# Performance work log

Measured on AMD Instinct MI355X. Metric: run time of the kernel, lower is better.

The kernel has to match this reference:

```python
import jax, jax.numpy as jnp
import numpy as np

B = 16384
N_NODES = 55
N = B * N_NODES
IN_CH = 13
HID = 32
MAX_NBR = 6
N_LAYERS = 5
E = 4 * N


def _sage(x, src, dst, wl, bl, wr, n):
    # PyG SAGEConv: out = lin_l(mean_j x_j) + lin_r(x_i); lin_l has bias, lin_r does not.
    msgs = x[src]                                                   # [E, d]
    agg = jax.ops.segment_sum(msgs, dst, num_segments=n)            # [N, d]
    cnt = jax.ops.segment_sum(jnp.ones((src.shape[0],), x.dtype), dst, num_segments=n)
    agg = agg / jnp.maximum(cnt, 1.0)[:, None]
    return agg @ wl + bl + x @ wr


def setup_inputs() -> dict:
    key = jax.random.key(0)
    ks = jax.random.split(key, 24)
    x = jax.random.normal(ks[0], (N, IN_CH), dtype=jnp.float32)
    # column -3 (index 10) is a binary neighbor mask: exactly MAX_NBR ones per graph
    u = jax.random.uniform(ks[1], (B, N_NODES))
    nbr_idx = jnp.argsort(u, axis=1)[:, :MAX_NBR]
    mask = jnp.zeros((B, N_NODES), jnp.float32).at[jnp.arange(B)[:, None], nbr_idx].set(1.0)
    x = x.at[:, IN_CH - 3].set(mask.reshape(-1))
    edge_index = jax.random.randint(ks[2], (2, E), 0, N, dtype=jnp.int64)
    shuffle_indices = jax.random.randint(ks[3], (B, MAX_NBR), 0, MAX_NBR, dtype=jnp.int64)
    s = 0.1
    wl0 = jax.random.normal(ks[4], (IN_CH, HID)) * s
    bl0 = jnp.zeros((HID,), jnp.float32)
    wr0 = jax.random.normal(ks[5], (IN_CH, HID)) * s
    wl = jax.random.normal(ks[6], (N_LAYERS - 1, HID, HID)) * s
    bl = jnp.zeros((N_LAYERS - 1, HID), jnp.float32)
    wr = jax.random.normal(ks[7], (N_LAYERS - 1, HID, HID)) * s
    wq = jax.random.normal(ks[8], (HID, HID)) * s
    bq = jnp.zeros((HID,), jnp.float32)
    wk = jax.random.normal(ks[9], (HID, HID)) * s
    bk = jnp.zeros((HID,), jnp.float32)
    wv = jax.random.normal(ks[10], (HID, HID)) * s
    bv = jnp.zeros((HID,), jnp.float32)
    wo = jax.random.normal(ks[11], (HID, HID)) * s
    bo = jnp.zeros((HID,), jnp.float32)
    w_fc = jax.random.normal(ks[12], (HID * MAX_NBR, MAX_NBR)) * s
    b_fc = jnp.zeros((MAX_NBR,), jnp.float32)
    return {"x": x, "edge_index": edge_index, "shuffle_indices": shuffle_indices,
            "wl0": wl0, "bl0": bl0, "wr0": wr0, "wl": wl, "bl": bl, "wr": wr,
            "wq": wq, "bq": bq, "wk": wk, "bk": bk, "wv": wv, "bv": bv,
            "wo": wo, "bo": bo, "w_fc": w_fc, "b_fc": b_fc}


def reference(x, edge_index, shuffle_indices, wl0, bl0, wr0, wl, bl, wr,
              wq, bq, wk, bk, wv, bv, wo, bo, w_fc, b_fc):
    n = x.shape[0]
    b = n // N_NODES
    src, dst = edge_index[0], edge_index[1]
    nbr_mask = x[:, IN_CH - 3].reshape(b, N_NODES)                  # [B, 55]

    h = jax.nn.selu(_sage(x, src, dst, wl0, bl0, wr0, n))
    jk = h
    for i in range(N_LAYERS - 1):
        h = jax.nn.selu(_sage(h, src, dst, wl[i], bl[i], wr[i], n))
        jk = jnp.maximum(jk, h)                                     # JumpingKnowledge('max')

    h = jax.nn.selu(jk)                                             # [N, HID]
    keys = h.reshape(b, N_NODES, HID)
    values = keys

    # dynamic neighbor gather: indices of mask==1 in ascending order, zero-padded to MAX_NBR
    order = jnp.argsort(-nbr_mask, axis=1, stable=True)[:, :MAX_NBR]  # [B, 6]
    barange = jnp.arange(b)[:, None]
    query = keys[barange, order]                                    # [B, 6, HID]
    valid = jnp.take_along_axis(nbr_mask, order, axis=1) > 0.5      # [B, 6] bool
    query = jnp.where(valid[..., None], query, 0.0)
    query = query[barange, shuffle_indices]                         # shuffled gather

    # single-head cross attention (head_dim = HID)
    Q = query @ wq + bq
    K = keys @ wk + bk
    V = values @ wv + bv
    scores = jnp.einsum('bqd,bkd->bqk', Q, K) / jnp.sqrt(jnp.float32(HID))
    attn = jax.nn.softmax(scores, axis=-1)
    out = jnp.einsum('bqk,bkd->bqd', attn, V) @ wo + bo             # [B, 6, HID]

    out = jax.nn.selu(out.reshape(b, HID * MAX_NBR))
    return out @ w_fc + b_fc                                        # [B, 6]
```

## Files before the change

### kernel.cpp

```cpp
#include <hip/hip_runtime.h>
#include <cstdint>
#include <cstddef>

#define NODES   55
#define BGRAPH  16384
#define NTOT    (BGRAPH*NODES)
#define INCH    13
#define HID     32
#define ETOT    (4*NTOT)
#define NPB     128
#define ECAP    768
#define ZN      NTOT

#define NBUCK   220
#define BSH     12
#define BMSK    4095
#define NBLK    2048
#define BCAP2   32
#define BINTH   256
#define BINGRP  (ETOT/4/NBLK)
#define OVFCAP  8192

#define ASTR    72
#define BSTR    72
#define ASTR0   40
#define WKV_OFF 9216

typedef _Float16 f16;
typedef _Float16 f16x4 __attribute__((ext_vector_type(4)));
typedef _Float16 f16x8 __attribute__((ext_vector_type(8)));
typedef float    f32x4 __attribute__((ext_vector_type(4)));

__device__ __forceinline__ float selu_f(float v){
  const float s  = 1.0507009873554805f;
  const float sa = 1.7580993408473766f;
  return v > 0.f ? s*v : sa*(__expf(v)-1.f);
}

__global__ __launch_bounds__(256) void k_pad(const float* __restrict__ x,
                                             float* __restrict__ xf,
                                             uint32_t* __restrict__ ha32,
                                             int* __restrict__ ocnt){
  if (blockIdx.x == 0){
    int t = threadIdx.x;
    if (t == 0) *ocnt = 0;
    if (t < 16)            xf[(size_t)ZN*16 + t] = 0.f;
    if (t >= 16 && t < 32) ha32[(size_t)ZN*16 + (t-16)] = 0u;
  }
  int i = blockIdx.x*256 + threadIdx.x;
  int node = i>>2, q = i&3;
  const float* r = x + (size_t)node*INCH + q*4;
  float4 v;
  v.x = r[0];
  v.y = (q<3) ? r[1] : 0.f;
  v.z = (q<3) ? r[2] : 0.f;
  v.w = (q<3) ? r[3] : 0.f;
  ((float4*)xf)[i] = v;
}

__global__ __launch_bounds__(256) void k_wprep(
    const float* __restrict__ wl0, const float* __restrict__ wr0,
    const float* __restrict__ wl,  const float* __restrict__ wr,
    const float* __restrict__ wk,  const float* __restrict__ wv,
    f16* __restrict__ wcp)
{
  int t = threadIdx.x;
  for (int i=t; i<1024; i+=256){
    int oc = i>>5, k = i&31;
    float v = 0.f;
    if (k < 13)                 v = wl0[k*HID + oc];
    else if (k >= 16 && k < 29) v = wr0[(k-16)*HID + oc];
    wcp[oc*32 + k] = (f16)v;
  }
  for (int i=t; i<4*2048; i+=256){
    int l = i>>11, r = i&2047, oc = r>>6, k = r&63;
    float v = (k<32) ? wl[l*1024 + k*HID + oc] : wr[l*1024 + (k-32)*HID + oc];
    wcp[1024 + l*2048 + oc*64 + k] = (f16)v;
  }
  for (int i=t; i<2048; i+=256){
    int oc = i>>5, k = i&31;
    float v = (oc < 32) ? wk[k*HID + oc] : wv[k*HID + (oc-32)];
    wcp[WKV_OFF + oc*32 + k] = (f16)v;
  }
}

__global__ __launch_bounds__(BINTH) void k_bin(
    const int* __restrict__ src, const int* __restrict__ dst,
    uint32_t* __restrict__ binned, int* __restrict__ gcnt,
    uint2* __restrict__ ovf, int* __restrict__ ocnt)
{
  __shared__ int lcnt[NBUCK];
  int t = threadIdx.x, bid = blockIdx.x;
  for (int i=t;i<NBUCK;i+=BINTH) lcnt[i]=0;
  __syncthreads();
  const int4* s4 = (const int4*)src;
  const int4* d4 = (const int4*)dst;
  int g0 = bid*BINGRP;
  for (int i=t; i<BINGRP; i+=BINTH){
    int4 s = s4[g0+i];
    int4 d = d4[g0+i];
    #pragma unroll
    for (int j=0;j<4;j++){
      int dd = (&d.x)[j];
      int ss = (&s.x)[j];
      int b  = dd >> BSH;
      uint32_t entry = (uint32_t)ss | ((uint32_t)(dd & BMSK) << 20);
      int pos = atomicAdd(&lcnt[b], 1);
      if (pos < BCAP2) binned[((size_t)b*NBLK + bid)*BCAP2 + pos] = entry;
      else {
        int gp = atomicAdd(ocnt, 1);
        if (gp < OVFCAP) ovf[gp] = make_uint2(entry, (uint32_t)b);
      }
    }
  }
  __syncthreads();
  for (int i=t;i<NBUCK;i+=BINTH){
    int c = lcnt[i]; if (c > BCAP2) c = BCAP2;
    gcnt[bid*NBUCK + i] = c;
  }
}

__global__ __launch_bounds__(256) void k_btot(const int* __restrict__ gcnt,
                                              const uint2* __restrict__ ovf,
                                              const int* __restrict__ ocnt,
                                              int* __restrict__ btot){
  __shared__ int sd[256];
  int b = blockIdx.x, t = threadIdx.x;
  int s = 0;
  for (int i=t;i<NBLK;i+=256) s += gcnt[i*NBUCK + b];
  int oc = *ocnt; if (oc > OVFCAP) oc = OVFCAP;
  for (int j=t;j<oc;j+=256) if (ovf[j].y == (uint32_t)b) s++;
  sd[t]=s; __syncthreads();
  for (int o=128;o>0;o>>=1){ if (t<o) sd[t]+=sd[t+o]; __syncthreads(); }
  if (t==0) btot[b]=sd[0];
}

__global__ __launch_bounds__(256) void k_bscan(const int* __restrict__ btot,
                                               int* __restrict__ bbase){
  __shared__ int sd[256];
  int t = threadIdx.x;
  int v = (t<NBUCK) ? btot[t] : 0;
  sd[t] = v; __syncthreads();
  for (int o=1;o<256;o<<=1){
    int u = (t>=o) ? sd[t-o] : 0;
    __syncthreads();
    sd[t] += u;
    __syncthreads();
  }
  if (t<NBUCK) bbase[t] = sd[t] - v;
}

__global__ __launch_bounds__(1024) void k_bucket(
    const uint32_t* __restrict__ binned, const int* __restrict__ gcnt,
    const int* __restrict__ bbase,
    const uint2* __restrict__ ovf, const int* __restrict__ ocnt,
    int* __restrict__ off, uint32_t* __restrict__ csrp)
{
  __shared__ int hist[4096];
  __shared__ int cnts[NBLK];
  __shared__ int ws[1024];
  int b = blockIdx.x, t = threadIdx.x;
  int base = bbase[b];
  for (int i=t;i<NBLK;i+=1024) cnts[i] = gcnt[i*NBUCK + b];
  #pragma unroll
  for (int i=0;i<4;i++) hist[t+1024*i] = 0;
  int oc = *ocnt; if (oc > OVFCAP) oc = OVFCAP;
  __syncthreads();

  const uint4* bb4 = (const uint4*)(binned + (size_t)b*(NBLK*BCAP2));
  for (int i=t; i<NBLK*BCAP2/4; i+=1024){
    uint4 e = bb4[i];
    int c = cnts[i>>3];
    int s0 = (i&7)*4;
    if (s0   < c) atomicAdd(&hist[(e.x>>20)&BMSK],1);
    if (s0+1 < c) atomicAdd(&hist[(e.y>>20)&BMSK],1);
    if (s0+2 < c) atomicAdd(&hist[(e.z>>20)&BMSK],1);
    if (s0+3 < c) atomicAdd(&hist[(e.w>>20)&BMSK],1);
  }
  for (int j=t;j<oc;j+=1024){
    uint2 pr = ovf[j];
    if (pr.y == (uint32_t)b) atomicAdd(&hist[(pr.x>>20)&BMSK],1);
  }
  __syncthreads();
  int t4 = t*4;
  int s0=hist[t4], s1=hist[t4+1], s2=hist[t4+2], s3=hist[t4+3];
  int sum = s0+s1+s2+s3;
  ws[t] = sum; __syncthreads();
  for (int o=1;o<1024;o<<=1){
    int u = (t>=o) ? ws[t-o] : 0;
    __syncthreads();
    ws[t] += u;
    __syncthreads();
  }
  int ex = ws[t] - sum;
  int p0 = ex, p1 = ex+s0, p2 = ex+s0+s1, p3 = ex+s0+s1+s2;
  hist[t4]=p0; hist[t4+1]=p1; hist[t4+2]=p2; hist[t4+3]=p3;
  int4 ov; ov.x = base+p0; ov.y = base+p1; ov.z = base+p2; ov.w = base+p3;
  ((int4*)(off + (b<<BSH)))[t] = ov;
  if (b == NBUCK-1 && t == 1023) off[NTOT] = ETOT;
  __syncthreads();
  for (int i=t; i<NBLK*BCAP2/4; i+=1024){
    uint4 e = bb4[i];
    int c = cnts[i>>3];
    int s0b = (i&7)*4;
    int p;
    if (s0b   < c){ p = atomicAdd(&hist[(e.x>>20)&BMSK],1); csrp[base+p] = e.x & 0xFFFFFu; }
    if (s0b+1 < c){ p = atomicAdd(&hist[(e.y>>20)&BMSK],1); csrp[base+p] = e.y & 0xFFFFFu; }
    if (s0b+2 < c){ p = atomicAdd(&hist[(e.z>>20)&BMSK],1); csrp[base+p] = e.z & 0xFFFFFu; }
    if (s0b+3 < c){ p = atomicAdd(&hist[(e.w>>20)&BMSK],1); csrp[base+p] = e.w & 0xFFFFFu; }
  }
  for (int j=t;j<oc;j+=1024){
    uint2 pr = ovf[j];
    if (pr.y == (uint32_t)b){
      int p = atomicAdd(&hist[(pr.x>>20)&BMSK],1);
      csrp[base+p] = pr.x & 0xFFFFFu;
    }
  }
}

__global__ __launch_bounds__(256,8) void k_layer0(
    const float* __restrict__ xf,
    const int* __restrict__ off, const uint32_t* __restrict__ csrp,
    const f16* __restrict__ wcat0, const float* __restrict__ bl0,
    f16* __restrict__ hout)
{
  __shared__ uint32_t ALDS[NPB*(ASTR0/2)];
  __shared__ uint32_t BLDS[32*(ASTR0/2)];
  __shared__ uint32_t EL[ECAP];
  __shared__ int      sOFF[NPB+2];
  __shared__ float    biasL[32];
  int t = threadIdx.x;
  int base = blockIdx.x*NPB;
  int e0 = off[base];
  int e1 = off[base+NPB];
  for (int i=t; i<NPB+1; i+=256) sOFF[i] = off[base+i];
  {
    int lim = (e1-e0) < ECAP ? (e1-e0) : ECAP;
    for (int i=t; i<lim; i+=256) EL[i] = csrp[e0+i];
  }
  if (t < 128){
    int oc = t>>2, kq = (t&3)*8;
    f16x8 wv = *(const f16x8*)(wcat0 + oc*32 + kq);
    *(f16x8*)((f16*)BLDS + oc*ASTR0 + kq) = wv;
  }
  if (t < 32) biasL[t] = bl0[t];
  __syncthreads();

  int c4 = t & 3;
  #pragma unroll
  for (int p=0;p<2;p++){
    int nl = p*64 + (t>>2);
    int node = base + nl;
    float4 xown = *((const float4*)(xf + (size_t)node*16) + c4);
    int s = sOFF[nl] - e0;
    int d = sOFF[nl+1] - sOFF[nl];
    float a0=0.f,a1=0.f,a2=0.f,a3=0.f;
    for (int i=0;i<d;i+=4){
      int j0 = s+i;
      uint32_t k0,k1,k2,k3;
      if (j0+3 < ECAP){ k0=EL[j0]; k1=EL[j0+1]; k2=EL[j0+2]; k3=EL[j0+3]; }
      else            { k0=csrp[e0+j0]; k1=csrp[e0+j0+1]; k2=csrp[e0+j0+2]; k3=csrp[e0+j0+3]; }
      k1 = (i+1<d)?k1:(uint32_t)ZN;
      k2 = (i+2<d)?k2:(uint32_t)ZN;
      k3 = (i+3<d)?k3:(uint32_t)ZN;
      float4 g0 = *((const float4*)(xf + (size_t)k0*16u) + c4);
      float4 g1 = *((const float4*)(xf + (size_t)k1*16u) + c4);
      float4 g2 = *((const float4*)(xf + (size_t)k2*16u) + c4);
      float4 g3 = *((const float4*)(xf + (size_t)k3*16u) + c4);
      a0 += (g0.x+g1.x)+(g2.x+g3.x);
      a1 += (g0.y+g1.y)+(g2.y+g3.y);
      a2 += (g0.z+g1.z)+(g2.z+g3.z);
      a3 += (g0.w+g1.w)+(g2.w+g3.w);
    }
    float inv = 1.f/(float)(d<1?1:d);
    union { f16 h[4]; uint32_t u[2]; } mp, xp;
    mp.h[0]=(f16)(a0*inv); mp.h[1]=(f16)(a1*inv); mp.h[2]=(f16)(a2*inv); mp.h[3]=(f16)(a3*inv);
    xp.h[0]=(f16)xown.x;   xp.h[1]=(f16)xown.y;   xp.h[2]=(f16)xown.z;   xp.h[3]=(f16)xown.w;
    uint32_t* arow = &ALDS[nl*(ASTR0/2)];
    *((uint2*)&arow[2*c4])     = make_uint2(mp.u[0], mp.u[1]);
    *((uint2*)&arow[8 + 2*c4]) = make_uint2(xp.u[0], xp.u[1]);
  }
  __syncthreads();

  int w = t>>6, l = t&63;
  int lrow = l&15, lg = l>>4;
  const f16* Af = (const f16*)ALDS;
  const f16* Bf = (const f16*)BLDS;
  f32x4 D00={0.f,0.f,0.f,0.f}, D01=D00, D10=D00, D11=D00;
  {
    f16x8 af0 = *(const f16x8*)(Af + (32*w+lrow)*ASTR0    + 8*lg);
    f16x8 af1 = *(const f16x8*)(Af + (32*w+16+lrow)*ASTR0 + 8*lg);
    f16x8 bf0 = *(const f16x8*)(Bf + lrow*ASTR0           + 8*lg);
    f16x8 bf1 = *(const f16x8*)(Bf + (16+lrow)*ASTR0      + 8*lg);
    D00 = __builtin_amdgcn_mfma_f32_16x16x32_f16(af0, bf0, D00, 0,0,0);
    D01 = __builtin_amdgcn_mfma_f32_16x16x32_f16(af0, bf1, D01, 0,0,0);
    D10 = __builtin_amdgcn_mfma_f32_16x16x32_f16(af1, bf0, D10, 0,0,0);
    D11 = __builtin_amdgcn_mfma_f32_16x16x32_f16(af1, bf1, D11, 0,0,0);
  }
  __syncthreads();

  f16* ST = (f16*)ALDS;
  #pragma unroll
  for (int j=0;j<4;j++){
    int r0 = 32*w + 4*lg + j, r1 = r0 + 16;
    ST[r0*34 + lrow]      = (f16)selu_f(D00[j] + biasL[lrow]);
    ST[r0*34 + 16 + lrow] = (f16)selu_f(D01[j] + biasL[16+lrow]);
    ST[r1*34 + lrow]      = (f16)selu_f(D10[j] + biasL[lrow]);
    ST[r1*34 + 16 + lrow] = (f16)selu_f(D11[j] + biasL[16+lrow]);
  }
  __syncthreads();

  const uint32_t* STd = (const uint32_t*)ALDS;
  uint4* ho4 = (uint4*)hout;
  int gbase = blockIdx.x*(NPB*HID/8);
  #pragma unroll
  for (int k=0;k<2;k++){
    int cch = t + 256*k;
    int n = cch>>2, m = cch&3;
    int dd = n*17 + m*4;
    uint4 u;
    u.x=STd[dd]; u.y=STd[dd+1]; u.z=STd[dd+2]; u.w=STd[dd+3];
    ho4[gbase+cch] = u;
  }
}

__global__ __launch_bounds__(256,6) void k_layer(
    const f16* __restrict__ hin,
    const int* __restrict__ off, const uint32_t* __restrict__ csrp,
    const f16* __restrict__ wcat, const float* __restrict__ bl,
    f16* __restrict__ hout, f16* __restrict__ jkio, int mode)
{
  __shared__ uint32_t ALDS[NPB*(ASTR/2)];
  __shared__ uint32_t BLDS[32*(BSTR/2)];
  __shared__ uint32_t EL[ECAP];
  __shared__ int      sOFF[NPB+2];
  __shared__ float    biasL[32];
  int t = threadIdx.x;
  int base = blockIdx.x*NPB;
  int e0 = off[base];
  int e1 = off[base+NPB];
  for (int i=t; i<NPB+1; i+=256) sOFF[i] = off[base+i];
  {
    int lim = (e1-e0) < ECAP ? (e1-e0) : ECAP;
    for (int i=t; i<lim; i+=256) EL[i] = csrp[e0+i];
  }
  if (t < 128){
    int oc = t>>2, kq = (t&3)*8;
    f16x8 wv0 = *(const f16x8*)(wcat + oc*64 + kq);
    f16x8 wv1 = *(const f16x8*)(wcat + oc*64 + 32 + kq);
    *(f16x8*)((f16*)BLDS + oc*BSTR + kq)      = wv0;
    *(f16x8*)((f16*)BLDS + oc*BSTR + 32 + kq) = wv1;
  }
  if (t < 32) biasL[t] = bl[t];
  __syncthreads();

  int c4 = t & 3;
  #pragma unroll
  for (int p=0;p<2;p++){
    int nl = p*64 + (t>>2);
    int node = base + nl;
    f16x8 hown = *(const f16x8*)(hin + (size_t)node*HID + 8u*c4);
    int s = sOFF[nl] - e0;
    int d = sOFF[nl+1] - sOFF[nl];
    float a[8];
    #pragma unroll
    for (int r=0;r<8;r++) a[r]=0.f;
    for (int i=0;i<d;i+=4){
      int j0 = s+i;
      uint32_t k0,k1,k2,k3;
      if (j0+3 < ECAP){ k0=EL[j0]; k1=EL[j0+1]; k2=EL[j0+2]; k3=EL[j0+3]; }
      else            { k0=csrp[e0+j0]; k1=csrp[e0+j0+1]; k2=csrp[e0+j0+2]; k3=csrp[e0+j0+3]; }
      k1 = (i+1<d)?k1:(uint32_t)ZN;
      k2 = (i+2<d)?k2:(uint32_t)ZN;
      k3 = (i+3<d)?k3:(uint32_t)ZN;
      f16x8 g0 = *((const f16x8*)(hin + (size_t)k0*32u) + c4);
      f16x8 g1 = *((const f16x8*)(hin + (size_t)k1*32u) + c4);
      f16x8 g2 = *((const f16x8*)(hin + (size_t)k2*32u) + c4);
      f16x8 g3 = *((const f16x8*)(hin + (size_t)k3*32u) + c4);
      #pragma unroll
      for (int r=0;r<8;r++)
        a[r] += ((float)g0[r]+(float)g1[r]) + ((float)g2[r]+(float)g3[r]);
    }
    float inv = 1.f/(float)(d<1?1:d);
    union { f16 h[8]; uint4 v; } mp;
    #pragma unroll
    for (int r=0;r<8;r++) mp.h[r] = (f16)(a[r]*inv);
    uint32_t* arow = &ALDS[nl*(ASTR/2)];
    *((uint4*)&arow[4*c4]) = mp.v;
    *((f16x8*)((f16*)arow + 32 + 8*c4)) = hown;
  }
  __syncthreads();

  int w = t>>6, l = t&63;
  int lrow = l&15, lg = l>>4;
  const f16* Af = (const f16*)ALDS;
  const f16* Bf = (const f16*)BLDS;
  f32x4 D00={0.f,0.f,0.f,0.f}, D01=D00, D10=D00, D11=D00;
  #pragma unroll
  for (int s2=0;s2<2;s2++){
    f16x8 af0 = *(const f16x8*)(Af + (32*w+lrow)*ASTR    + 32*s2 + 8*lg);
    f16x8 af1 = *(const f16x8*)(Af + (32*w+16+lrow)*ASTR + 32*s2 + 8*lg);
    f16x8 bf0 = *(const f16x8*)(Bf + lrow*BSTR           + 32*s2 + 8*lg);
    f16x8 bf1 = *(const f16x8*)(Bf + (16+lrow)*BSTR      + 32*s2 + 8*lg);
    D00 = __builtin_amdgcn_mfma_f32_16x16x32_f16(af0, bf0, D00, 0,0,0);
    D01 = __builtin_amdgcn_mfma_f32_16x16x32_f16(af0, bf1, D01, 0,0,0);
    D10 = __builtin_amdgcn_mfma_f32_16x16x32_f16(af1, bf0, D10, 0,0,0);
    D11 = __builtin_amdgcn_mfma_f32_16x16x32_f16(af1, bf1, D11, 0,0,0);
  }
  __syncthreads();

  f16* ST = (f16*)ALDS;
  #pragma unroll
  for (int j=0;j<4;j++){
    int r0 = 32*w + 4*lg + j, r1 = r0 + 16;
    ST[r0*34 + lrow]      = (f16)selu_f(D00[j] + biasL[lrow]);
    ST[r0*34 + 16 + lrow] = (f16)selu_f(D01[j] + biasL[16+lrow]);
    ST[r1*34 + lrow]      = (f16)selu_f(D10[j] + biasL[lrow]);
    ST[r1*34 + 16 + lrow] = (f16)selu_f(D11[j] + biasL[16+lrow]);
  }
  __syncthreads();

  const uint32_t* STd = (const uint32_t*)ALDS;
  uint4* ho4 = (uint4*)hout;
  uint4* jo4 = (uint4*)jkio;
  const uint4* hi4 = (const uint4*)hin;
  int gbase = blockIdx.x*(NPB*HID/8);
  #pragma unroll
  for (int k=0;k<2;k++){
    int cch = t + 256*k;
    int n = cch>>2, m = cch&3;
    int dd = n*17 + m*4;
    union { uint4 u; f16 hh[8]; } hv, jv;
    hv.u.x=STd[dd]; hv.u.y=STd[dd+1]; hv.u.z=STd[dd+2]; hv.u.w=STd[dd+3];
    jv.u = (mode == 0) ? hi4[gbase+cch] : jo4[gbase+cch];
    #pragma unroll
    for (int r=0;r<8;r++){
      f16 a = jv.hh[r], b = hv.hh[r];
      jv.hh[r] = (b > a) ? b : a;
    }
    if (mode != 2) ho4[gbase+cch] = hv.u;
    jo4[gbase+cch] = jv.u;
  }
}

__global__ __launch_bounds__(256) void k_attn(
    const f16* __restrict__ jk, const float* __restrict__ x,
    const int* __restrict__ shuf, const f16* __restrict__ wkvT,
    const float* __restrict__ wq, const float* __restrict__ bq,
    const float* __restrict__ bk, const float* __restrict__ bv,
    const float* __restrict__ wo, const float* __restrict__ bo,
    const float* __restrict__ wfc, const float* __restrict__ bfc,
    float* __restrict__ out)
{
  __shared__ alignas(16) f16 Ah[64*40];
  __shared__ float K[NODES*33];
  __shared__ float V[NODES*33];
  __shared__ float Qs[6*33];
  __shared__ float S[6*56];
  __shared__ float O[6*33];
  __shared__ float SO[192];
  __shared__ float part[96];
  __shared__ int   sel[8];

  int g = blockIdx.x, t = threadIdx.x;

  {
    const f16x8* j8 = (const f16x8*)(jk + (size_t)g*NODES*HID);
    for (int i=t; i<NODES*HID/8; i+=256){
      f16x8 v = j8[i];
      int node = i >> 2, c0 = (i & 3)*8;
      f16x8 hv;
      #pragma unroll
      for (int r=0;r<8;r++) hv[r] = (f16)selu_f((float)v[r]);
      *(f16x8*)(Ah + node*40 + c0) = hv;
    }
  }
  if (t < 64){
    float mv = (t < NODES) ? x[(size_t)(g*NODES+t)*INCH + (INCH-3)] : 0.f;
    unsigned long long mb = __ballot(mv > 0.5f);
    if (t < 6){
      int kk = shuf[g*6 + t];
      for (int i2=0;i2<kk;i2++) mb &= (mb - 1ull);
      sel[t] = (int)__builtin_ctzll(mb);
    }
  }
  __syncthreads();

  {
    int w = t>>6, l = t&63;
    int lrow = l&15, lg = l>>4;
    f16x8 af = *(const f16x8*)(Ah + (16*w + lrow)*40 + 8*lg);
    #pragma unroll
    for (int ct=0; ct<4; ct++){
      f16x8 bf = *(const f16x8*)(wkvT + (16*ct + lrow)*32 + 8*lg);
      f32x4 D = {0.f,0.f,0.f,0.f};
      D = __builtin_amdgcn_mfma_f32_16x16x32_f16(af, bf, D, 0,0,0);
      int ocl = 16*(ct&1) + lrow;
      float bias = (ct < 2) ? bk[ocl] : bv[ocl];
      float* dst = (ct < 2) ? K : V;
      #pragma unroll
      for (int j=0;j<4;j++){
        int node = 16*w + 4*lg + j;
        if (node < NODES) dst[node*33 + ocl] = D[j] + bias;
      }
    }
  }
  if (t < 192){
    int q = t>>5, oc = t&31;
    int node = sel[q];
    const f16x8* hr8 = (const f16x8*)(Ah + node*40);
    float a = bq[oc];
    #pragma unroll
    for (int cc=0;cc<4;cc++){
      f16x8 hv = hr8[cc];
      #pragma unroll
      for (int r=0;r<8;r++) a = fmaf((float)hv[r], wq[(8*cc+r)*HID + oc], a);
    }
    Qs[q*33+oc] = a;
  }
  __syncthreads();

  for (int idx=t; idx<6*NODES; idx+=256){
    int q = idx % 6, k = idx / 6;
    float a = 0.f;
    #pragma unroll
    for (int c=0;c<HID;c++) a = fmaf(Qs[q*33+c], K[k*33+c], a);
    S[q*56+k] = a * 0.17677669529663687f;
  }
  __syncthreads();

  if (t < 192){
    int q = t>>5, l = t&31;
    float v0 = (l      < NODES) ? S[q*56+l]    : -1e30f;
    float v1 = (l+32   < NODES) ? S[q*56+l+32] : -1e30f;
    float mx = fmaxf(v0, v1);
    #pragma unroll
    for (int o=16;o>0;o>>=1) mx = fmaxf(mx, __shfl_xor(mx, o, 32));
    float p0 = (l    < NODES) ? __expf(v0-mx) : 0.f;
    float p1 = (l+32 < NODES) ? __expf(v1-mx) : 0.f;
    float sm = p0 + p1;
    #pragma unroll
    for (int o=16;o>0;o>>=1) sm += __shfl_xor(sm, o, 32);
    float inv = 1.f/sm;
    if (l    < NODES) S[q*56+l]    = p0*inv;
    if (l+32 < NODES) S[q*56+l+32] = p1*inv;
  }
  __syncthreads();

  if (t < 192){
    int q = t>>5, oc = t&31;
    float a = 0.f;
    for (int k=0;k<NODES;k++) a = fmaf(S[q*56+k], V[k*33+oc], a);
    O[q*33+oc] = a;
  }
  __syncthreads();

  if (t < 192){
    int q = t>>5, oc = t&31;
    float a = bo[oc];
    #pragma unroll
    for (int c=0;c<HID;c++) a = fmaf(O[q*33+c], wo[c*HID+oc], a);
    SO[t] = selu_f(a);
  }
  __syncthreads();

  if (t < 96){
    int j = t % 6, pp = t / 6;
    float a = 0.f;
    #pragma unroll
    for (int r=0;r<12;r++) a = fmaf(SO[pp*12+r], wfc[(pp*12+r)*6+j], a);
    part[pp*6+j] = a;
  }
  __syncthreads();
  if (t < 6){
    float a = bfc[t];
    #pragma unroll
    for (int pp=0;pp<16;pp++) a += part[pp*6+t];
    out[g*6+t] = a;
  }
}

extern "C" void kernel_launch(void* const* d_in, const int* in_sizes, int n_in,
                              void* d_out, int out_size, void* d_ws, size_t ws_size,
                              hipStream_t stream)
{
  const float* x   = (const float*)d_in[0];
  const int*   eix = (const int*)d_in[1];
  const int*   shf = (const int*)d_in[2];
  const float* wl0 = (const float*)d_in[3];
  const float* bl0 = (const float*)d_in[4];
  const float* wr0 = (const float*)d_in[5];
  const float* wl  = (const float*)d_in[6];
  const float* bl  = (const float*)d_in[7];
  const float* wr  = (const float*)d_in[8];
  const float* wq  = (const float*)d_in[9];
  const float* bq  = (const float*)d_in[10];
  const float* wk  = (const float*)d_in[11];
  const float* bk  = (const float*)d_in[12];
  const float* wv  = (const float*)d_in[13];
  const float* bv  = (const float*)d_in[14];
  const float* wo  = (const float*)d_in[15];
  const float* bo  = (const float*)d_in[16];
  const float* wfc = (const float*)d_in[17];
  const float* bfc = (const float*)d_in[18];
  float* out = (float*)d_out;

  const int* esrc = eix;
  const int* edst = eix + ETOT;

  char* p = (char*)d_ws;
  auto carve = [&](size_t bytes){ void* r = (void*)p; p += (bytes + 255) & ~(size_t)255; return r; };
  int*      off   = (int*)carve(sizeof(int)*(NTOT+1));
  int*      gcnt  = (int*)carve(sizeof(int)*(size_t)NBLK*NBUCK);
  int*      btot  = (int*)carve(sizeof(int)*256);
  int*      bbase = (int*)carve(sizeof(int)*256);
  uint2*    ovf   = (uint2*)carve(sizeof(uint2)*OVFCAP);
  int*      ocnt  = (int*)carve(sizeof(int)*64);
  f16*      wcp   = (f16*)carve(sizeof(f16)*(WKV_OFF + 2048));
  uint32_t* csrp  = (uint32_t*)carve(sizeof(uint32_t)*((size_t)ETOT + 64));
  f16*      h_a   = (f16*)carve(2*((size_t)NTOT+1)*HID);
  f16*      h_b   = (f16*)carve(2*((size_t)NTOT+1)*HID);
  f16*      jk16  = (f16*)carve(2*(size_t)NTOT*HID);

  float*    xf     = (float*)h_b;
  uint32_t* binned = (uint32_t*)h_a;

  k_pad   <<<ETOT/256,  256, 0, stream>>>(x, xf, (uint32_t*)h_a, ocnt);
  k_wprep <<<1,         256, 0, stream>>>(wl0, wr0, wl, wr, wk, wv, wcp);
  k_bin   <<<NBLK,    BINTH, 0, stream>>>(esrc, edst, binned, gcnt, ovf, ocnt);
  k_btot  <<<NBUCK,     256, 0, stream>>>(gcnt, ovf, ocnt, btot);
  k_bscan <<<1,         256, 0, stream>>>(btot, bbase);
  k_bucket<<<NBUCK,    1024, 0, stream>>>(binned, gcnt, bbase, ovf, ocnt, off, csrp);

  k_layer0<<<NTOT/NPB, 256, 0, stream>>>(xf, off, csrp, wcp, bl0, h_a);
  f16* hc = h_a; f16* hn = h_b;
  for (int l=0; l<4; l++){
    int mode = (l == 0) ? 0 : ((l == 3) ? 2 : 1);
    k_layer<<<NTOT/NPB, 256, 0, stream>>>(hc, off, csrp,
                                          wcp + 1024 + l*2048, bl + l*HID,
                                          hn, jk16, mode);
    f16* tmp = hc; hc = hn; hn = tmp;
  }
  k_attn<<<BGRAPH, 256, 0, stream>>>(jk16, x, shf, wcp + WKV_OFF,
                                     wq, bq, bk, bv, wo, bo, wfc, bfc, out);
}
```

Baseline: 824.6 us.

## Store layer-0 input features in fp16 and skip one jumping-knowledge read-modify-write pass

Padded input features are now stored as fp16 instead of fp32, which halves the bytes moved by the random neighbor gathers in layer 0. The jumping-knowledge max is restructured: layer 1 no longer reads or writes the jk buffer, and layer 2 folds in the previous layer's output from the hin buffer, saving a full read and write of the jk array. Jk accesses also switch to nontemporal loads and stores. In exchange, inputs are quantised to fp16 earlier and the correctness depends on the ping-pong buffer still holding layer-1 output when layer 2 runs.

```diff
diff --git a/kernel.cpp b/kernel.cpp
--- a/kernel.cpp
+++ b/kernel.cpp
@@ -26,10 +26,16 @@
 #define ASTR0   40
 #define WKV_OFF 9216
 
+#define MODE_A  0
+#define MODE_D  2
+#define MODE_B  3
+#define MODE_C  4
+
 typedef _Float16 f16;
 typedef _Float16 f16x4 __attribute__((ext_vector_type(4)));
 typedef _Float16 f16x8 __attribute__((ext_vector_type(8)));
 typedef float    f32x4 __attribute__((ext_vector_type(4)));
+typedef uint32_t u32x4 __attribute__((ext_vector_type(4)));
 
 __device__ __forceinline__ float selu_f(float v){
   const float s  = 1.0507009873554805f;
@@ -38,24 +44,26 @@
 }
 
 __global__ __launch_bounds__(256) void k_pad(const float* __restrict__ x,
-                                             float* __restrict__ xf,
-                                             uint32_t* __restrict__ ha32,
+                                             f16* __restrict__ xh,
+                                             f16* __restrict__ ha,
+                                             f16* __restrict__ hb,
                                              int* __restrict__ ocnt){
   if (blockIdx.x == 0){
     int t = threadIdx.x;
     if (t == 0) *ocnt = 0;
-    if (t < 16)            xf[(size_t)ZN*16 + t] = 0.f;
-    if (t >= 16 && t < 32) ha32[(size_t)ZN*16 + (t-16)] = 0u;
+    if (t < 16)                  xh[(size_t)ZN*16 + t]      = (f16)0.f;
+    else if (t >= 16 && t < 48)  ha[(size_t)ZN*32 + (t-16)] = (f16)0.f;
+    else if (t >= 48 && t < 80)  hb[(size_t)ZN*32 + (t-48)] = (f16)0.f;
   }
   int i = blockIdx.x*256 + threadIdx.x;
   int node = i>>2, q = i&3;
   const float* r = x + (size_t)node*INCH + q*4;
-  float4 v;
-  v.x = r[0];
-  v.y = (q<3) ? r[1] : 0.f;
-  v.z = (q<3) ? r[2] : 0.f;
-  v.w = (q<3) ? r[3] : 0.f;
-  ((float4*)xf)[i] = v;
+  f16x4 v;
+  v[0] = (f16)r[0];
+  v[1] = (q<3) ? (f16)r[1] : (f16)0.f;
+  v[2] = (q<3) ? (f16)r[2] : (f16)0.f;
+  v[3] = (q<3) ? (f16)r[3] : (f16)0.f;
+  *(f16x4*)(xh + (size_t)node*16 + q*4) = v;
 }
 
 __global__ __launch_bounds__(256) void k_wprep(
@@ -219,7 +227,7 @@
 }
 
 __global__ __launch_bounds__(256,8) void k_layer0(
-    const float* __restrict__ xf,
+    const f16* __restrict__ xh,
     const int* __restrict__ off, const uint32_t* __restrict__ csrp,
     const f16* __restrict__ wcat0, const float* __restrict__ bl0,
     f16* __restrict__ hout)
@@ -251,7 +259,7 @@
   for (int p=0;p<2;p++){
     int nl = p*64 + (t>>2);
     int node = base + nl;
-    float4 xown = *((const float4*)(xf + (size_t)node*16) + c4);
+    f16x4 xown = *(const f16x4*)(xh + (size_t)node*16 + 4u*c4);
     int s = sOFF[nl] - e0;
     int d = sOFF[nl+1] - sOFF[nl];
     float a0=0.f,a1=0.f,a2=0.f,a3=0.f;
@@ -263,19 +271,19 @@
       k1 = (i+1<d)?k1:(uint32_t)ZN;
       k2 = (i+2<d)?k2:(uint32_t)ZN;
       k3 = (i+3<d)?k3:(uint32_t)ZN;
-      float4 g0 = *((const float4*)(xf + (size_t)k0*16u) + c4);
-      float4 g1 = *((const float4*)(xf + (size_t)k1*16u) + c4);
-      float4 g2 = *((const float4*)(xf + (size_t)k2*16u) + c4);
-      float4 g3 = *((const float4*)(xf + (size_t)k3*16u) + c4);
-      a0 += (g0.x+g1.x)+(g2.x+g3.x);
-      a1 += (g0.y+g1.y)+(g2.y+g3.y);
-      a2 += (g0.z+g1.z)+(g2.z+g3.z);
-      a3 += (g0.w+g1.w)+(g2.w+g3.w);
+      f16x4 g0 = *(const f16x4*)(xh + (size_t)k0*16u + 4u*c4);
+      f16x4 g1 = *(const f16x4*)(xh + (size_t)k1*16u + 4u*c4);
+      f16x4 g2 = *(const f16x4*)(xh + (size_t)k2*16u + 4u*c4);
+      f16x4 g3 = *(const f16x4*)(xh + (size_t)k3*16u + 4u*c4);
+      a0 += ((float)g0[0]+(float)g1[0]) + ((float)g2[0]+(float)g3[0]);
+      a1 += ((float)g0[1]+(float)g1[1]) + ((float)g2[1]+(float)g3[1]);
+      a2 += ((float)g0[2]+(float)g1[2]) + ((float)g2[2]+(float)g3[2]);
+      a3 += ((float)g0[3]+(float)g1[3]) + ((float)g2[3]+(float)g3[3]);
     }
     float inv = 1.f/(float)(d<1?1:d);
     union { f16 h[4]; uint32_t u[2]; } mp, xp;
     mp.h[0]=(f16)(a0*inv); mp.h[1]=(f16)(a1*inv); mp.h[2]=(f16)(a2*inv); mp.h[3]=(f16)(a3*inv);
-    xp.h[0]=(f16)xown.x;   xp.h[1]=(f16)xown.y;   xp.h[2]=(f16)xown.z;   xp.h[3]=(f16)xown.w;
+    xp.h[0]=xown[0]; xp.h[1]=xown[1]; xp.h[2]=xown[2]; xp.h[3]=xown[3];
     uint32_t* arow = &ALDS[nl*(ASTR0/2)];
     *((uint2*)&arow[2*c4])     = make_uint2(mp.u[0], mp.u[1]);
     *((uint2*)&arow[8 + 2*c4]) = make_uint2(xp.u[0], xp.u[1]);
@@ -421,25 +429,31 @@
   __syncthreads();
 
   const uint32_t* STd = (const uint32_t*)ALDS;
-  uint4* ho4 = (uint4*)hout;
-  uint4* jo4 = (uint4*)jkio;
-  const uint4* hi4 = (const uint4*)hin;
+  u32x4* ho4 = (u32x4*)hout;
+  u32x4* jo4 = (u32x4*)jkio;
+  const u32x4* hi4 = (const u32x4*)hin;
   int gbase = blockIdx.x*(NPB*HID/8);
   #pragma unroll
   for (int k=0;k<2;k++){
     int cch = t + 256*k;
     int n = cch>>2, m = cch&3;
     int dd = n*17 + m*4;
-    union { uint4 u; f16 hh[8]; } hv, jv;
-    hv.u.x=STd[dd]; hv.u.y=STd[dd+1]; hv.u.z=STd[dd+2]; hv.u.w=STd[dd+3];
-    jv.u = (mode == 0) ? hi4[gbase+cch] : jo4[gbase+cch];
-    #pragma unroll
-    for (int r=0;r<8;r++){
-      f16 a = jv.hh[r], b = hv.hh[r];
-      jv.hh[r] = (b > a) ? b : a;
-    }
-    if (mode != 2) ho4[gbase+cch] = hv.u;
-    jo4[gbase+cch] = jv.u;
+    union UU { u32x4 u; f16 hh[8]; };
+    UU hv, jv, j2;
+    hv.u = (u32x4){STd[dd], STd[dd+1], STd[dd+2], STd[dd+3]};
+    if (mode != MODE_B){
+      if (mode == MODE_A) jv.u = hi4[gbase+cch];
+      else                jv.u = __builtin_nontemporal_load(jo4 + gbase + cch);
+      if (mode == MODE_C){
+        j2.u = hi4[gbase+cch];
+        #pragma unroll
+        for (int r=0;r<8;r++) jv.hh[r] = (j2.hh[r] > jv.hh[r]) ? j2.hh[r] : jv.hh[r];
+      }
+      #pragma unroll
+      for (int r=0;r<8;r++) jv.hh[r] = (hv.hh[r] > jv.hh[r]) ? hv.hh[r] : jv.hh[r];
+      __builtin_nontemporal_store(jv.u, jo4 + gbase + cch);
+    }
+    if (mode != MODE_D) ho4[gbase+cch] = hv.u;
   }
 }
 
@@ -467,7 +481,7 @@
   {
     const f16x8* j8 = (const f16x8*)(jk + (size_t)g*NODES*HID);
     for (int i=t; i<NODES*HID/8; i+=256){
-      f16x8 v = j8[i];
+      f16x8 v = __builtin_nontemporal_load(j8 + i);
       int node = i >> 2, c0 = (i & 3)*8;
       f16x8 hv;
       #pragma unroll
@@ -622,23 +636,23 @@
   f16*      h_b   = (f16*)carve(2*((size_t)NTOT+1)*HID);
   f16*      jk16  = (f16*)carve(2*(size_t)NTOT*HID);
 
-  float*    xf     = (float*)h_b;
+  f16*      xh     = (f16*)h_b;
   uint32_t* binned = (uint32_t*)h_a;
 
-  k_pad   <<<ETOT/256,  256, 0, stream>>>(x, xf, (uint32_t*)h_a, ocnt);
+  k_pad   <<<ETOT/256,  256, 0, stream>>>(x, xh, h_a, h_b, ocnt);
   k_wprep <<<1,         256, 0, stream>>>(wl0, wr0, wl, wr, wk, wv, wcp);
   k_bin   <<<NBLK,    BINTH, 0, stream>>>(esrc, edst, binned, gcnt, ovf, ocnt);
   k_btot  <<<NBUCK,     256, 0, stream>>>(gcnt, ovf, ocnt, btot);
   k_bscan <<<1,         256, 0, stream>>>(btot, bbase);
   k_bucket<<<NBUCK,    1024, 0, stream>>>(binned, gcnt, bbase, ovf, ocnt, off, csrp);
 
-  k_layer0<<<NTOT/NPB, 256, 0, stream>>>(xf, off, csrp, wcp, bl0, h_a);
+  k_layer0<<<NTOT/NPB, 256, 0, stream>>>(xh, off, csrp, wcp, bl0, h_a);
   f16* hc = h_a; f16* hn = h_b;
+  static const int modes[4] = {MODE_A, MODE_B, MODE_C, MODE_D};
   for (int l=0; l<4; l++){
-    int mode = (l == 0) ? 0 : ((l == 3) ? 2 : 1);
     k_layer<<<NTOT/NPB, 256, 0, stream>>>(hc, off, csrp,
                                           wcp + 1024 + l*2048, bl + l*HID,
-                                          hn, jk16, mode);
+                                          hn, jk16, modes[l]);
     f16* tmp = hc; hc = hn; hn = tmp;
   }
   k_attn<<<BGRAPH, 256, 0, stream>>>(jk16, x, shf, wcp + WKV_OFF,
```

New measurement: 811.3 us. No clear change (-1.6%).
